# Performance work log

Measured on AMD Instinct MI355X. Metric: run time of the kernel, lower is better.

## Reference

```python
import jax, jax.numpy as jnp
import numpy as np

# Static module configuration (matches init_kwargs)
B, CIN, COUT, K, H, W = 4, 32, 32, 3, 128, 128
UM = 2                      # um_dim: 2D vector fields
NW = ((K - 1) // 2) * 4     # num_weights = radius*4 = 4


def setup_inputs() -> dict:
    key = jax.random.key(0)
    k1, k2, k3 = jax.random.split(key, 3)
    params = jax.random.normal(k1, (COUT, CIN, NW, 4), jnp.float32)
    basis = jax.random.normal(k2, (NW, 4, K, K, UM, UM), jnp.float32)
    # Replicate the init-time scaling of the torch module:
    # std over the (non-zero) outer-product kernel, then scale params and basis.
    init_kernel = jnp.einsum('abcd,cdefgh->abcdefgh', params, basis)
    stds = jnp.std(init_kernel)  # random basis -> all entries nonzero
    scaler = jnp.sqrt(0.6 / (np.sqrt(CIN) * (K ** 2) * stds))
    params = params * scaler
    basis = basis * scaler
    bias_term = jnp.ones((1, COUT, 2, 1, 1), jnp.float32) / 100.0
    b = jnp.float32(0.01)
    xx = jax.random.normal(k3, (B, CIN * UM, H, W), jnp.float32)
    return {'xx': xx, 'params': params, 'basis': basis,
            'bias_term': bias_term, 'b': b}


def _forward(xx, params, basis, bias_term, b):
    Bn, C, Hh, Ww = xx.shape
    I, O = CIN, COUT
    # --- get_kernel: einsum + transposes -> conv weight (O*2, I*2, K, K) ---
    Kr = jnp.einsum('abcd,cdefgh->abefgh', params, basis)      # (O,I,K,K,2,2)
    kernel = jnp.transpose(Kr, (0, 4, 1, 5, 2, 3)).reshape(O * 2, I * 2, K, K)
    # --- unfold with replicate padding: P[b,c,kh,kw,h,w] ---
    xp = jnp.pad(xx, ((0, 0), (0, 0), (1, 1), (1, 1)), mode='edge')
    P = jnp.stack([xp[:, :, i:i + Hh, j:j + Ww]
                   for i in range(K) for j in range(K)], axis=2)
    P = P.reshape(Bn, C, K, K, Hh, Ww)
    # --- per-window mean subtraction over (input_channels, kh, kw) ---
    P5 = P.reshape(Bn, I, UM, K, K, Hh, Ww)
    avgs = P5.mean(axis=(1, 3, 4), keepdims=True)              # (B,1,2,1,1,H,W)
    P = (P5 - avgs).reshape(Bn, C, K, K, Hh, Ww)
    avgs = avgs[:, :, :, 0, 0]                                 # (B,1,2,H,W)
    # --- strided conv2d on the blown-up grid == this einsum:
    # big[b,c,3h+di,3w+dj] = P[b,c,kh=dj,kw=di,h,w], so kernel (di,dj)=(p,q)
    # pairs with patch (kh=q, kw=p).
    out = jnp.einsum('bcqphw,ocpq->bohw', P, kernel)           # (B,O*2,H,W)
    out = out.reshape(Bn, O, 2, Hh, Ww) + bias_term
    # --- 'relu' vector activation: normalize, zero where norm <= b ---
    norm = jnp.sqrt(out[:, :, 0] ** 2 + out[:, :, 1] ** 2)[:, :, None]
    out = jnp.where(norm - b <= 0.0, 0.0, out / norm)
    # --- add_mean ---
    out = out + avgs
    return out.reshape(Bn, O * 2, Hh, Ww)


def reference(xx, params, basis, bias_term, b):
    return _forward(xx, params, basis, bias_term, b)
```

## Files before the change

kernel.cpp:

```cpp
#include <hip/hip_runtime.h>

#define BN 4
#define CH 64
#define HH 128
#define WW 128
#define PIX (HH*WW)

#define OFF_WL  0
#define OFF_S   36864
#define OFF_CS  36992

#define SR 12
#define SCH (10*SR)
#define NCELL 100
#define NSTAGE (8*NCELL)

__device__ __forceinline__ int iclamp(int v, int lo, int hi) {
    return v < lo ? lo : (v > hi ? hi : v);
}

__global__ __launch_bounds__(256) void k_prep(const float* __restrict__ params,
                                              const float* __restrict__ basis,
                                              const float* __restrict__ x,
                                              float* __restrict__ Wl,
                                              float* __restrict__ S,
                                              float* __restrict__ cs) {
    int bx = blockIdx.x;
    if (bx < 144) {
        int idx = bx * 256 + threadIdx.x;
        int oc  = idx & 63;
        int tap = (idx >> 6) % 9;
        int c   = idx / 576;
        int q = tap / 3, p = tap % 3;
        int o = oc >> 1, g = oc & 1;
        int i = c >> 1, u = c & 1;
        float s = 0.f;
        #pragma unroll
        for (int n = 0; n < 4; ++n)
            #pragma unroll
            for (int d = 0; d < 4; ++d)
                s = fmaf(params[((o * 32 + i) * 4 + n) * 4 + d],
                         basis[((((n * 4 + d) * 3 + p) * 3 + q) * 2 + g) * 2 + u], s);
        Wl[(((oc >> 4) * 64 + c) * 9 + tap) * 16 + (oc & 15)] = s;
    } else if (bx == 144) {
        int t = threadIdx.x;
        if (t < 128) {
            int u = t >> 6, oc = t & 63;
            int o = oc >> 1, g = oc & 1;
            float s = 0.f;
            #pragma unroll
            for (int nd = 0; nd < 16; ++nd) {
                int n = nd >> 2, d = nd & 3;
                float pa = 0.f;
                for (int i = 0; i < 32; ++i)
                    pa += params[((o * 32 + i) * 4 + n) * 4 + d];
                float sb = 0.f;
                #pragma unroll
                for (int e = 0; e < 3; ++e)
                    #pragma unroll
                    for (int f = 0; f < 3; ++f)
                        sb += basis[((((n * 4 + d) * 3 + e) * 3 + f) * 2 + g) * 2 + u];
                s = fmaf(pa, sb, s);
            }
            S[t] = s;
        }
    } else {
        int idx = (bx - 145) * 256 + threadIdx.x;
        int pq  = idx & (PIX / 4 - 1);
        int u   = (idx >> 12) & 1;
        int b   = idx >> 13;
        const float4* xb = (const float4*)x;
        float4 s = make_float4(0.f, 0.f, 0.f, 0.f);
        #pragma unroll
        for (int i = 0; i < 32; ++i) {
            float4 v = xb[(size_t)(b * CH + 2 * i + u) * (PIX / 4) + pq];
            s.x += v.x; s.y += v.y; s.z += v.z; s.w += v.w;
        }
        ((float4*)cs)[(b * 2 + u) * (PIX / 4) + pq] = s;
    }
}

__global__ __launch_bounds__(64, 4) void k_main(
    const float* __restrict__ x,
    const float* __restrict__ Wl,
    const float* __restrict__ S,
    const float* __restrict__ bias,
    const float* __restrict__ cs,
    const float* __restrict__ bptr,
    float* __restrict__ out)
{
    __shared__ float sm[8 * SCH];

    int tile = blockIdx.x;
    int ocg  = blockIdx.y;
    int b    = blockIdx.z;
    int tid = threadIdx.x;
    int py = tid >> 3, px = tid & 7;
    int h0 = (tile >> 4) * 8, w0 = (tile & 15) * 8;
    int h = h0 + py, w = w0 + px;

    const float* xb = x + (size_t)b * CH * PIX;

    int goff[13], loff[13];
    #pragma unroll
    for (int k = 0; k < 13; ++k) {
        int cell = tid + (k << 6);
        if (cell >= NSTAGE) cell = NSTAGE - 1;
        int cc = cell / NCELL;
        int r  = cell - cc * NCELL;
        int hy = r / 10, hx = r - (r / 10) * 10;
        int gy = iclamp(h0 - 1 + hy, 0, HH - 1);
        int gx = iclamp(w0 - 1 + hx, 0, WW - 1);
        goff[k] = cc * PIX + gy * WW + gx;
        loff[k] = cc * SCH + hy * SR + hx;
    }
    bool act12 = tid < (NSTAGE - 768);
    int lrd = py * SR + px;

    float acc[16];
    #pragma unroll
    for (int j = 0; j < 16; ++j) acc[j] = 0.f;

    #pragma unroll
    for (int k = 0; k < 12; ++k) sm[loff[k]] = xb[goff[k]];
    if (act12) sm[loff[12]] = xb[goff[12]];
    __syncthreads();

    const float* wbase = Wl + (size_t)ocg * 64 * 144;

    for (int c0 = 0; c0 < CH; c0 += 8) {
        float xf[13];
        bool more = (c0 + 8 < CH);
        if (more) {
            const float* xn = xb + (size_t)(c0 + 8) * PIX;
            #pragma unroll
            for (int k = 0; k < 12; ++k) xf[k] = xn[goff[k]];
            if (act12) xf[12] = xn[goff[12]];
        }

        const float* wc = wbase + c0 * 144;
        #pragma unroll
        for (int cc = 0; cc < 8; ++cc) {
            float xv[9];
            #pragma unroll
            for (int dy = 0; dy < 3; ++dy)
                #pragma unroll
                for (int dx = 0; dx < 3; ++dx)
                    xv[dy * 3 + dx] = sm[lrd + cc * SCH + dy * SR + dx];
            const float* wt = wc + cc * 144;
            #pragma unroll
            for (int t = 0; t < 9; ++t) {
                float xt = xv[t];
                #pragma unroll
                for (int j = 0; j < 16; ++j)
                    acc[j] = fmaf(xt, wt[t * 16 + j], acc[j]);
            }
        }

        if (more) {
            __syncthreads();
            #pragma unroll
            for (int k = 0; k < 12; ++k) sm[loff[k]] = xf[k];
            if (act12) sm[loff[12]] = xf[12];
            __syncthreads();
        }
    }

    int pix = h * WW + w;
    int hm = h > 0 ? h - 1 : 0, hp = h < HH - 1 ? h + 1 : HH - 1;
    int wm = w > 0 ? w - 1 : 0, wp = w < WW - 1 ? w + 1 : WW - 1;
    const float* c0p = cs + (size_t)(b * 2 + 0) * PIX;
    const float* c1p = cs + (size_t)(b * 2 + 1) * PIX;
    int r0 = hm * WW, r1 = h * WW, r2 = hp * WW;
    float a0 = (c0p[r0 + wm] + c0p[r0 + w] + c0p[r0 + wp]
              + c0p[r1 + wm] + c0p[r1 + w] + c0p[r1 + wp]
              + c0p[r2 + wm] + c0p[r2 + w] + c0p[r2 + wp]) * (1.0f / 288.0f);
    float a1 = (c1p[r0 + wm] + c1p[r0 + w] + c1p[r0 + wp]
              + c1p[r1 + wm] + c1p[r1 + w] + c1p[r1 + wp]
              + c1p[r2 + wm] + c1p[r2 + w] + c1p[r2 + wp]) * (1.0f / 288.0f);
    float bthr = bptr[0];

    float* ob = out + (size_t)b * CH * PIX + pix;
    #pragma unroll
    for (int j = 0; j < 16; j += 2) {
        int oc = ocg * 16 + j;
        float t0 = acc[j]     - a0 * S[oc]     - a1 * S[64 + oc]     + bias[oc];
        float t1 = acc[j + 1] - a0 * S[oc + 1] - a1 * S[64 + oc + 1] + bias[oc + 1];
        float n = sqrtf(t0 * t0 + t1 * t1);
        float r0v, r1v;
        if (n - bthr <= 0.f) { r0v = 0.f; r1v = 0.f; }
        else { r0v = t0 / n; r1v = t1 / n; }
        ob[(size_t)oc * PIX]       = r0v + a0;
        ob[(size_t)(oc + 1) * PIX] = r1v + a1;
    }
}

extern "C" void kernel_launch(void* const* d_in, const int* in_sizes, int n_in,
                              void* d_out, int out_size, void* d_ws, size_t ws_size,
                              hipStream_t stream) {
    const float* xx     = (const float*)d_in[0];
    const float* params = (const float*)d_in[1];
    const float* basis  = (const float*)d_in[2];
    const float* bias   = (const float*)d_in[3];
    const float* bptr   = (const float*)d_in[4];
    float* out = (float*)d_out;
    float* ws  = (float*)d_ws;

    float* Wl  = ws + OFF_WL;
    float* S   = ws + OFF_S;
    float* cs  = ws + OFF_CS;

    k_prep<<<273, 256, 0, stream>>>(params, basis, xx, Wl, S, cs);

    dim3 grid(256, 4, BN);
    k_main<<<grid, 64, 0, stream>>>(xx, Wl, S, bias, cs, bptr, out);
}
```

Baseline: 147.0 us.

## Replace shared-memory halo staging with direct register-prefetched global loads on larger tiles

Removes the LDS staging of 8-channel halo tiles and the barriers that went with it. Each thread now reads its own 9 neighbour values per channel straight from global memory, with a two-channel register double-buffer that prefetches the next pair while FMAs run. Blocks grow from 64 to 256 threads, each covering a 16x16 pixel tile, so there are fewer blocks and weights are reused across more pixels per block. The cost is that neighbouring threads load overlapping values redundantly and rely on L1/L2 to absorb it, and register pressure rises with the prefetch buffers.

```diff
diff --git a/kernel.cpp b/kernel.cpp
--- a/kernel.cpp
+++ b/kernel.cpp
@@ -9,11 +9,6 @@
 #define OFF_WL  0
 #define OFF_S   36864
 #define OFF_CS  36992
-
-#define SR 12
-#define SCH (10*SR)
-#define NCELL 100
-#define NSTAGE (8*NCELL)
 
 __device__ __forceinline__ int iclamp(int v, int lo, int hi) {
     return v < lo ? lo : (v > hi ? hi : v);
@@ -80,7 +75,7 @@
     }
 }
 
-__global__ __launch_bounds__(64, 4) void k_main(
+__global__ __launch_bounds__(256, 4) void k_main(
     const float* __restrict__ x,
     const float* __restrict__ Wl,
     const float* __restrict__ S,
@@ -89,89 +84,72 @@
     const float* __restrict__ bptr,
     float* __restrict__ out)
 {
-    __shared__ float sm[8 * SCH];
-
     int tile = blockIdx.x;
     int ocg  = blockIdx.y;
     int b    = blockIdx.z;
-    int tid = threadIdx.x;
-    int py = tid >> 3, px = tid & 7;
-    int h0 = (tile >> 4) * 8, w0 = (tile & 15) * 8;
-    int h = h0 + py, w = w0 + px;
+    int ty = threadIdx.x >> 4, tx = threadIdx.x & 15;
+    int h = (tile >> 3) * 16 + ty;
+    int w = (tile & 7) * 16 + tx;
 
-    const float* xb = x + (size_t)b * CH * PIX;
-
-    int goff[13], loff[13];
+    int hm = h > 0 ? h - 1 : 0, hp = h < HH - 1 ? h + 1 : HH - 1;
+    int wm = w > 0 ? w - 1 : 0, wp = w < WW - 1 ? w + 1 : WW - 1;
+    int rowoff[3] = { hm * WW, h * WW, hp * WW };
+    int coloff[3] = { wm, w, wp };
+    int off[9];
     #pragma unroll
-    for (int k = 0; k < 13; ++k) {
-        int cell = tid + (k << 6);
-        if (cell >= NSTAGE) cell = NSTAGE - 1;
-        int cc = cell / NCELL;
-        int r  = cell - cc * NCELL;
-        int hy = r / 10, hx = r - (r / 10) * 10;
-        int gy = iclamp(h0 - 1 + hy, 0, HH - 1);
-        int gx = iclamp(w0 - 1 + hx, 0, WW - 1);
-        goff[k] = cc * PIX + gy * WW + gx;
-        loff[k] = cc * SCH + hy * SR + hx;
-    }
-    bool act12 = tid < (NSTAGE - 768);
-    int lrd = py * SR + px;
+    for (int r = 0; r < 3; ++r)
+        #pragma unroll
+        for (int p = 0; p < 3; ++p)
+            off[r * 3 + p] = rowoff[r] + coloff[p];
 
     float acc[16];
     #pragma unroll
     for (int j = 0; j < 16; ++j) acc[j] = 0.f;
 
+    const float* xb = x + (size_t)b * CH * PIX;
+    const float* wc = Wl + (size_t)ocg * 64 * 144;
+
+    float xA[9], xB[9];
     #pragma unroll
-    for (int k = 0; k < 12; ++k) sm[loff[k]] = xb[goff[k]];
-    if (act12) sm[loff[12]] = xb[goff[12]];
-    __syncthreads();
+    for (int k = 0; k < 9; ++k) xA[k] = xb[off[k]];
+    #pragma unroll
+    for (int k = 0; k < 9; ++k) xB[k] = xb[PIX + off[k]];
 
-    const float* wbase = Wl + (size_t)ocg * 64 * 144;
+    for (int c = 0; c < CH; c += 2) {
+        int c2 = c + 2 < CH ? c + 2 : CH - 1;
+        int c3 = c + 3 < CH ? c + 3 : CH - 1;
+        const float* p2 = xb + (size_t)c2 * PIX;
+        const float* p3 = xb + (size_t)c3 * PIX;
+        float xN0[9], xN1[9];
+        #pragma unroll
+        for (int k = 0; k < 9; ++k) xN0[k] = p2[off[k]];
+        #pragma unroll
+        for (int k = 0; k < 9; ++k) xN1[k] = p3[off[k]];
 
-    for (int c0 = 0; c0 < CH; c0 += 8) {
-        float xf[13];
-        bool more = (c0 + 8 < CH);
-        if (more) {
-            const float* xn = xb + (size_t)(c0 + 8) * PIX;
+        #pragma unroll
+        for (int t = 0; t < 9; ++t) {
+            float xt = xA[t];
             #pragma unroll
-            for (int k = 0; k < 12; ++k) xf[k] = xn[goff[k]];
-            if (act12) xf[12] = xn[goff[12]];
+            for (int j = 0; j < 16; ++j)
+                acc[j] = fmaf(xt, wc[t * 16 + j], acc[j]);
+        }
+        #pragma unroll
+        for (int t = 0; t < 9; ++t) {
+            float xt = xB[t];
+            #pragma unroll
+            for (int j = 0; j < 16; ++j)
+                acc[j] = fmaf(xt, wc[144 + t * 16 + j], acc[j]);
         }
 
-        const float* wc = wbase + c0 * 144;
         #pragma unroll
-        for (int cc = 0; cc < 8; ++cc) {
-            float xv[9];
-            #pragma unroll
-            for (int dy = 0; dy < 3; ++dy)
-                #pragma unroll
-                for (int dx = 0; dx < 3; ++dx)
-                    xv[dy * 3 + dx] = sm[lrd + cc * SCH + dy * SR + dx];
-            const float* wt = wc + cc * 144;
-            #pragma unroll
-            for (int t = 0; t < 9; ++t) {
-                float xt = xv[t];
-                #pragma unroll
-                for (int j = 0; j < 16; ++j)
-                    acc[j] = fmaf(xt, wt[t * 16 + j], acc[j]);
-            }
-        }
-
-        if (more) {
-            __syncthreads();
-            #pragma unroll
-            for (int k = 0; k < 12; ++k) sm[loff[k]] = xf[k];
-            if (act12) sm[loff[12]] = xf[12];
-            __syncthreads();
-        }
+        for (int k = 0; k < 9; ++k) { xA[k] = xN0[k]; xB[k] = xN1[k]; }
+        wc += 288;
     }
 
     int pix = h * WW + w;
-    int hm = h > 0 ? h - 1 : 0, hp = h < HH - 1 ? h + 1 : HH - 1;
-    int wm = w > 0 ? w - 1 : 0, wp = w < WW - 1 ? w + 1 : WW - 1;
     const float* c0p = cs + (size_t)(b * 2 + 0) * PIX;
     const float* c1p = cs + (size_t)(b * 2 + 1) * PIX;
-    int r0 = hm * WW, r1 = h * WW, r2 = hp * WW;
+    int r0 = rowoff[0], r1 = rowoff[1], r2 = rowoff[2];
     float a0 = (c0p[r0 + wm] + c0p[r0 + w] + c0p[r0 + wp]
               + c0p[r1 + wm] + c0p[r1 + w] + c0p[r1 + wp]
               + c0p[r2 + wm] + c0p[r2 + w] + c0p[r2 + wp]) * (1.0f / 288.0f);
@@ -212,6 +190,6 @@
 
     k_prep<<<273, 256, 0, stream>>>(params, basis, xx, Wl, S, cs);
 
-    dim3 grid(256, 4, BN);
-    k_main<<<grid, 64, 0, stream>>>(xx, Wl, S, bias, cs, bptr, out);
+    dim3 grid(64, 4, BN);
+    k_main<<<grid, 256, 0, stream>>>(xx, Wl, S, bias, cs, bptr, out);
 }
```

Result: no change. 144.7 us (-1.6%).
